# Performance work log

Measured on AMD Instinct MI355X. Metric: run time of the kernel, lower is better.

## Reference

```python
import jax, jax.numpy as jnp
import numpy as np
from jax import lax


def _conv(x, w, b=None):
    # NCHW conv, 'same' padding, stride 1
    y = lax.conv_general_dilated(x, w, (1, 1), 'SAME',
                                 dimension_numbers=('NCHW', 'OIHW', 'NCHW'))
    return y if b is None else y + b[None, :, None, None]


def _up2(x):
    # nn.Upsample(scale_factor=2), nearest
    return jnp.repeat(jnp.repeat(x, 2, axis=2), 2, axis=3)


def _rot_attn(x, wq, wk, wv, lng, lnb, reach=1):
    # Batched sliding-window rotatory cross-attention (replaces the Python loop
    # over window positions).  x: [B, C, H, W]; each position i in [reach, B-reach)
    # attends (as query) to its 2*reach neighbor frames.
    B, C, H, W = x.shape
    xs = x.reshape(B, C, H * W).transpose(0, 2, 1)          # [B, N, C]
    tgt = xs[reach:B - reach]                               # [P, N, C]
    offs = [o for o in range(-reach, reach + 1) if o != 0]  # fixed small set
    nbs = jnp.stack([xs[reach + o: B - reach + o] for o in offs], axis=1)  # [P,2r,N,C]
    q = tgt @ wq
    k = nbs @ wk
    v = nbs @ wv
    scores = jnp.einsum('pnc,pjmc->pjnm', q, k) / jnp.asarray(C, x.dtype) ** 0.5
    ctx = jnp.einsum('pjnm,pjmc->pjnc', jax.nn.softmax(scores, axis=-1), v).mean(1)  # [P,N,C]
    # LayerNorm over C
    mu = ctx.mean(-1, keepdims=True)
    var = ((ctx - mu) ** 2).mean(-1, keepdims=True)
    ctx = (ctx - mu) * lax.rsqrt(var + 1e-5) * lng + lnb
    cm = ctx.mean(0)                                        # mean over positions [N,C]
    return x + cm.T.reshape(C, H, W)[None]                  # broadcast residual


def _block(h, skip, w_up, b_up, wq, wk, wv, lng, lnb, bng, bnb, w_cb):
    h = _conv(_up2(h), w_up, b_up)                          # 1x1 conv
    h = jnp.concatenate([h, skip], axis=1)
    h = _rot_attn(h, wq, wk, wv, lng, lnb)
    # ConvolutionBatchNormblock: BN (batch stats, eps=1e-5) -> ReLU -> conv (no bias)
    mu = h.mean((0, 2, 3))
    var = ((h - mu[None, :, None, None]) ** 2).mean((0, 2, 3))
    h = (h - mu[None, :, None, None]) * lax.rsqrt(var + 1e-5)[None, :, None, None]
    h = h * bng[None, :, None, None] + bnb[None, :, None, None]
    return _conv(jax.nn.relu(h), w_cb)


def setup_inputs() -> dict:
    key = jax.random.key(0)
    ks = iter(jax.random.split(key, 64))
    n = lambda shape, s: jax.random.normal(next(ks), shape, jnp.float32) * s
    d = {}
    d['x'] = n([6, 64, 768], 1.0)
    d['skip0'] = n([6, 256, 16, 16], 1.0)
    d['skip1'] = n([6, 128, 32, 32], 1.0)
    d['skip2'] = n([6, 64, 64, 64], 1.0)
    d['w_sc'] = n([512, 768, 3, 3], 0.02)
    d['b_sc'] = jnp.zeros([512], jnp.float32)
    for i, (cin, cout) in enumerate([(512, 256), (256, 128), (128, 64)], 1):
        s = cin ** -0.5
        d[f'w_up{i}'] = n([cout, cin, 1, 1], s)
        d[f'b_up{i}'] = jnp.zeros([cout], jnp.float32)
        d[f'wq{i}'] = n([cin, cin], s)
        d[f'wk{i}'] = n([cin, cin], s)
        d[f'wv{i}'] = n([cin, cin], s)
        d[f'lng{i}'] = jnp.ones([cin], jnp.float32)
        d[f'lnb{i}'] = jnp.zeros([cin], jnp.float32)
        d[f'bng{i}'] = jnp.ones([cin], jnp.float32)
        d[f'bnb{i}'] = jnp.zeros([cin], jnp.float32)
        d[f'w_cb{i}'] = n([cout, cin, 3, 3], s * 0.3)
    return d


def reference(x, skip0, skip1, skip2, w_sc, b_sc,
              w_up1, b_up1, wq1, wk1, wv1, lng1, lnb1, bng1, bnb1, w_cb1,
              w_up2, b_up2, wq2, wk2, wv2, lng2, lnb2, bng2, bnb2, w_cb2,
              w_up3, b_up3, wq3, wk3, wv3, lng3, lnb3, bng3, bnb3, w_cb3):
    B, N, D = x.shape
    g = int(N ** 0.5)  # 8x8 token grid (image_size*2 / patch_size)
    h = _conv(x.transpose(0, 2, 1).reshape(B, D, g, g), w_sc, b_sc)   # [B,512,8,8]
    h = _block(h, skip0, w_up1, b_up1, wq1, wk1, wv1, lng1, lnb1, bng1, bnb1, w_cb1)
    h = _block(h, skip1, w_up2, b_up2, wq2, wk2, wv2, lng2, lnb2, bng2, bnb2, w_cb2)
    h = _block(h, skip2, w_up3, b_up3, wq3, wk3, wv3, lng3, lnb3, bng3, bnb3, w_cb3)
    return _up2(h)                                                    # [B,64,128,128]
```

## Files before the change

### kernel.cpp

```cpp
#include <hip/hip_runtime.h>
#include <hip/hip_bf16.h>

typedef const float* fp;
typedef unsigned short u16;
typedef __attribute__((ext_vector_type(8))) short short8v;
typedef __attribute__((ext_vector_type(4))) float f32x4;

__device__ __forceinline__ u16 f2b(float f){
  union{float f; unsigned u;} x; x.f = f;
  unsigned r = x.u + 0x7FFFu + ((x.u>>16)&1u);
  return (u16)(r>>16);
}

__global__ __launch_bounds__(256) void k_fill(float* out, int n, float v){
  int i = blockIdx.x*256 + threadIdx.x;
  if(i < n) out[i] = v;
}
__global__ __launch_bounds__(256) void k_fillb(float* out, fp bias, int Cout, int N){
  int i = blockIdx.x*256 + threadIdx.x;
  if(i < 6*Cout*N) out[i] = bias[(i/N)%Cout];
}
__global__ __launch_bounds__(256) void k_b16(fp in, u16* o, int n){
  int i = (blockIdx.x*256 + threadIdx.x)*8;
  if(i >= n) return;
  u16 tmp[8];
  #pragma unroll
  for(int e=0;e<8;e++) tmp[e] = f2b(in[i+e]);
  *(short8v*)(o+i) = *(const short8v*)tmp;
}
__global__ __launch_bounds__(256) void k_wtr(fp w, u16* wt, int Cout, int Cin){
  int idx = blockIdx.x*256 + threadIdx.x;
  int cc = Cout*Cin;
  if(idx >= 9*cc) return;
  int tap = idx / cc, rem = idx - tap*cc;
  wt[idx] = f2b(w[(size_t)rem*9 + tap]);
}
__global__ __launch_bounds__(256) void k_wqkvt(fp wq, fp wk, fp wv, u16* bt, int C, float rs){
  int idx = blockIdx.x*256 + threadIdx.x;
  if(idx >= 3*C*C) return;
  int r = idx / C, ci = idx - r*C;
  int sel = r / C, co = r - sel*C;
  float v = (sel==0 ? wq : sel==1 ? wk : wv)[(size_t)ci*C + co];
  bt[idx] = f2b(sel==0 ? v*rs : v);
}

__global__ __launch_bounds__(256) void k_in_tr(fp x, float* h0){
  int n = blockIdx.x, b = blockIdx.y;
  for(int d = threadIdx.x; d < 768; d += blockDim.x)
    h0[((size_t)b*768 + d)*64 + n] = x[((size_t)b*64 + n)*768 + d];
}

__global__ __launch_bounds__(256) void k_conv3_mfma2(const u16* __restrict__ wt,
    const u16* __restrict__ inb16, float* __restrict__ out,
    int Cin, int Cout, int H, int W, int S){
  const int N = H*W;
  __shared__ u16 As[64*40];
  __shared__ u16 Bs[64*40];
  int t = threadIdx.x, wid = t>>6, lane = t&63, l15 = lane&15, g = lane>>4;
  int b = blockIdx.z / S, s = blockIdx.z % S;
  int co0 = blockIdx.y*64, px0 = blockIdx.x*64;
  int ciN = Cin/S, ci0 = s*ciN;
  const u16* inb = inb16 + (size_t)b*Cin*N;
  int arow = t>>2, acol = (t&3)*8;
  int bpx = t&63, boct = t>>6;
  int p = px0 + bpx, py = p/W, px_ = p - py*W;
  int nc = ciN >> 5, nk = 9*nc;
  f32x4 acc[4];
  #pragma unroll
  for(int i=0;i<4;i++) acc[i] = f32x4{0.f,0.f,0.f,0.f};
  short8v av; u16 bt[8];

  #define PREF(ks) { int tap = (ks)/nc; int c0 = ((ks) - tap*nc)<<5;                     \
      int dy = tap/3 - 1, dx = tap - (tap/3)*3 - 1;                                      \
      av = *(const short8v*)(wt + ((size_t)tap*Cout + co0 + arow)*Cin + ci0 + c0 + acol);\
      bool val = ((unsigned)(py+dy) < (unsigned)H) && ((unsigned)(px_+dx) < (unsigned)W);\
      const u16* bp = inb + (size_t)(ci0 + c0 + boct*8)*N + (p + dy*W + dx);             \
      _Pragma("unroll") for(int e=0;e<8;e++) bt[e] = val ? bp[(size_t)e*N] : (u16)0; }

  PREF(0);
  for(int ks = 0; ks < nk; ks++){
    __syncthreads();
    *(short8v*)(As + arow*40 + acol) = av;
    *(short8v*)(Bs + bpx*40 + boct*8) = *(const short8v*)bt;
    __syncthreads();
    if(ks+1 < nk) PREF(ks+1);
    short8v a = *(const short8v*)(As + (wid*16+l15)*40 + 8*g);
    #pragma unroll
    for(int pt=0; pt<4; pt++){
      short8v bf = *(const short8v*)(Bs + (pt*16+l15)*40 + 8*g);
      acc[pt] = __builtin_amdgcn_mfma_f32_16x16x32_bf16(a, bf, acc[pt], 0,0,0);
    }
  }
  #undef PREF
  #pragma unroll
  for(int pt=0; pt<4; pt++){
    #pragma unroll
    for(int r=0; r<4; r++){
      size_t o = ((size_t)b*Cout + co0 + wid*16 + 4*g + r)*N + px0 + pt*16 + l15;
      if(S == 1) out[o] = acc[pt][r];
      else atomicAdd(out + o, acc[pt][r]);
    }
  }
}

__global__ __launch_bounds__(256) void k_gemm_qkv(const u16* __restrict__ XB,
    const u16* __restrict__ BT, u16* __restrict__ Qo, u16* __restrict__ Ko,
    u16* __restrict__ Vo, int C, int Nn){
  __shared__ u16 As[64*40], Bs[64*40];
  int t = threadIdx.x, wid = t>>6, lane = t&63, l15 = lane&15, g = lane>>4;
  int r0 = blockIdx.x*64, c0 = blockIdx.y*64;
  int arow = t>>2, acol = (t&3)*8;
  int nk = C/32;
  f32x4 acc[4];
  #pragma unroll
  for(int i=0;i<4;i++) acc[i] = f32x4{0.f,0.f,0.f,0.f};
  short8v av = *(const short8v*)(XB + (size_t)(r0+arow)*C + acol);
  short8v bv = *(const short8v*)(BT + (size_t)(c0+arow)*C + acol);
  for(int ks = 0; ks < nk; ks++){
    __syncthreads();
    *(short8v*)(As + arow*40 + acol) = av;
    *(short8v*)(Bs + arow*40 + acol) = bv;
    __syncthreads();
    if(ks+1 < nk){
      int k0 = (ks+1)*32;
      av = *(const short8v*)(XB + (size_t)(r0+arow)*C + k0 + acol);
      bv = *(const short8v*)(BT + (size_t)(c0+arow)*C + k0 + acol);
    }
    short8v a = *(const short8v*)(As + (wid*16+l15)*40 + 8*g);
    #pragma unroll
    for(int pt=0; pt<4; pt++){
      short8v bf = *(const short8v*)(Bs + (pt*16+l15)*40 + 8*g);
      acc[pt] = __builtin_amdgcn_mfma_f32_16x16x32_bf16(a, bf, acc[pt], 0,0,0);
    }
  }
  int sel = c0 / C, cb = c0 - sel*C;
  if(sel < 2){
    u16* ob = sel==0 ? Qo : Ko;
    #pragma unroll
    for(int pt=0; pt<4; pt++){
      #pragma unroll
      for(int r=0; r<4; r++)
        ob[(size_t)(r0 + wid*16 + 4*g + r)*C + cb + pt*16 + l15] = f2b(acc[pt][r]);
    }
  }else{
    int b = r0 / Nn, nb = r0 - b*Nn;
    #pragma unroll
    for(int pt=0; pt<4; pt++){
      #pragma unroll
      for(int r=0; r<4; r++)
        Vo[((size_t)b*C + cb + pt*16 + l15)*Nn + nb + wid*16 + 4*g + r] = f2b(acc[pt][r]);
    }
  }
}

__global__ void k_conv1_low(const float* __restrict__ in, fp w, fp bias,
                            float* __restrict__ out, int Cin, int Cout, int N1){
  int bc = blockIdx.x; int b = bc / Cout; int co = bc % Cout;
  extern __shared__ float ws[];
  for(int i = threadIdx.x; i < Cin; i += blockDim.x) ws[i] = w[(size_t)co*Cin + i];
  __syncthreads();
  const float* inb = in + (size_t)b*Cin*N1;
  float bv = bias[co];
  for(int p = threadIdx.x; p < N1; p += blockDim.x){
    float acc = bv;
    for(int ci = 0; ci < Cin; ci++) acc += inb[(size_t)ci*N1 + p] * ws[ci];
    out[((size_t)b*Cout + co)*N1 + p] = acc;
  }
}

__global__ __launch_bounds__(256) void k_concat_up(const float* __restrict__ a, fp skip,
                                                   float* __restrict__ cat,
                                                   int Ca, int Cs, int N2, int W2){
  int bc = blockIdx.x; int C = Ca + Cs; int b = bc / C; int c = bc % C;
  float* o = cat + (size_t)bc*N2;
  if(c < Ca){
    const float* s = a + ((size_t)b*Ca + c)*(N2/4);
    int W1 = W2/2;
    for(int n = threadIdx.x; n < N2; n += blockDim.x){
      int y = n / W2, x = n % W2;
      o[n] = s[(y>>1)*W1 + (x>>1)];
    }
  }else{
    fp s = skip + ((size_t)b*Cs + (c-Ca))*N2;
    for(int n = threadIdx.x; n < N2; n += blockDim.x) o[n] = s[n];
  }
}

__global__ __launch_bounds__(256) void k_trb(const float* __restrict__ src, u16* __restrict__ dst,
                                             int C, int N){
  __shared__ float tb[32][33];
  int b = blockIdx.z;
  int c0 = blockIdx.y*32, n0 = blockIdx.x*32;
  int tx = threadIdx.x & 31, ty = threadIdx.x >> 5;
  for(int i = ty; i < 32; i += 8) tb[i][tx] = src[((size_t)b*C + c0+i)*N + n0+tx];
  __syncthreads();
  for(int i = ty; i < 32; i += 8) dst[((size_t)b*N + n0+i)*C + c0+tx] = f2b(tb[tx][i]);
}

__global__ __launch_bounds__(256) void k_attn128(const u16* __restrict__ Q,
                                                 const u16* __restrict__ K,
                                                 const u16* __restrict__ VT,
                                                 float* __restrict__ ctxn, int N){
  constexpr int C = 128, KVB = 64, KP = C+8, VP = KVB+8;
  __shared__ u16 Ks[KVB*KP];
  __shared__ u16 Vt[C*VP];
  __shared__ u16 ps[4][16*VP];
  int t = threadIdx.x, wid = t>>6, lane = t&63, l15 = lane&15, g = lane>>4;
  int p = blockIdx.y, q0 = (blockIdx.x*4 + wid)*16, j = blockIdx.z;
  const u16* Qb = Q + ((size_t)(p+1)*N + q0)*C;
  const u16* Kb = K  + (size_t)(p + (j?2:0))*N*C;
  const u16* Vb = VT + (size_t)(p + (j?2:0))*C*N;
  short8v qf[4];
  #pragma unroll
  for(int kk = 0; kk < 4; kk++)
    qf[kk] = *(const short8v*)(Qb + (size_t)l15*C + kk*32 + 8*g);
  f32x4 acc[8];
  #pragma unroll
  for(int i=0;i<8;i++) acc[i] = f32x4{0.f,0.f,0.f,0.f};
  float m[4] = {-1e30f,-1e30f,-1e30f,-1e30f};
  float l[4] = {0.f,0.f,0.f,0.f};
  short8v kpre[4], vpre[4];

  #define APREF(M0) { _Pragma("unroll") for(int i=0;i<4;i++){                  \
        int idx = t*8 + i*2048; int mm = idx>>7, cc = idx&127;                 \
        kpre[i] = *(const short8v*)(Kb + (size_t)((M0)+mm)*C + cc); }          \
      _Pragma("unroll") for(int i=0;i<4;i++){                                  \
        int idx = t*8 + i*2048; int c = idx>>6, mo = idx&63;                   \
        vpre[i] = *(const short8v*)(Vb + (size_t)c*N + (M0) + mo); } }

  APREF(0);
  for(int m0 = 0; m0 < N; m0 += KVB){
    __syncthreads();
    #pragma unroll
    for(int i=0;i<4;i++){ int idx = t*8 + i*2048; int mm = idx>>7, cc = idx&127;
      *(short8v*)(Ks + mm*KP + cc) = kpre[i]; }
    #pragma unroll
    for(int i=0;i<4;i++){ int idx = t*8 + i*2048; int c = idx>>6, mo = idx&63;
      *(short8v*)(Vt + c*VP + mo) = vpre[i]; }
    __syncthreads();
    if(m0 + KVB < N) APREF(m0 + KVB);
    f32x4 s[4];
    #pragma unroll
    for(int h=0; h<4; h++){
      s[h] = f32x4{0.f,0.f,0.f,0.f};
      #pragma unroll
      for(int kk=0; kk<4; kk++){
        short8v kf = *(const short8v*)(Ks + (h*16+l15)*KP + kk*32 + 8*g);
        s[h] = __builtin_amdgcn_mfma_f32_16x16x32_bf16(qf[kk], kf, s[h], 0,0,0);
      }
    }
    float pmax[4]; bool need = false;
    #pragma unroll
    for(int r=0; r<4; r++){
      float mx = fmaxf(fmaxf(s[0][r],s[1][r]), fmaxf(s[2][r],s[3][r]));
      #pragma unroll
      for(int off=1; off<16; off<<=1) mx = fmaxf(mx, __shfl_xor(mx, off));
      pmax[r] = mx; need |= (mx > m[r] + 8.f);
    }
    if(__any((int)need)){
      #pragma unroll
      for(int r=0; r<4; r++){
        float mnew = fmaxf(m[r], pmax[r]);
        float scl = __expf(m[r] - mnew);
        l[r] *= scl; m[r] = mnew;
        #pragma unroll
        for(int ct=0; ct<8; ct++) acc[ct][r] *= scl;
      }
    }
    #pragma unroll
    for(int r=0; r<4; r++){
      float psum = 0.f;
      #pragma unroll
      for(int h=0; h<4; h++){
        float e = __expf(s[h][r] - m[r]); psum += e;
        ps[wid][(4*g+r)*VP + h*16 + l15] = f2b(e);
      }
      #pragma unroll
      for(int off=1; off<16; off<<=1) psum += __shfl_xor(psum, off);
      l[r] += psum;
    }
    #pragma unroll
    for(int ks=0; ks<2; ks++){
      short8v pa = *(const short8v*)(ps[wid] + l15*VP + ks*32 + 8*g);
      #pragma unroll
      for(int ct=0; ct<8; ct++){
        short8v vb = *(const short8v*)(Vt + (ct*16+l15)*VP + ks*32 + 8*g);
        acc[ct] = __builtin_amdgcn_mfma_f32_16x16x32_bf16(pa, vb, acc[ct], 0,0,0);
      }
    }
  }
  #undef APREF
  float inv[4];
  #pragma unroll
  for(int r=0; r<4; r++) inv[r] = 0.5f/l[r];
  #pragma unroll
  for(int ct=0; ct<8; ct++){
    int c = ct*16 + l15;
    #pragma unroll
    for(int r=0; r<4; r++)
      atomicAdd(&ctxn[((size_t)p*N + q0 + 4*g + r)*C + c], acc[ct][r]*inv[r]);
  }
}

template<int C>
__global__ __launch_bounds__(256) void k_attn_mfma(const u16* __restrict__ Q,
                                                   const u16* __restrict__ K,
                                                   const u16* __restrict__ VT,
                                                   float* __restrict__ ctxn, int N){
  constexpr int KP = C + 8;
  __shared__ u16 Ks[32*KP];
  __shared__ u16 Vt[C*40];
  __shared__ u16 ps[4][16*40];
  int t = threadIdx.x, wid = t>>6, lane = t&63;
  int l15 = lane&15, g = lane>>4;
  int p = blockIdx.y, j = blockIdx.z;
  int q0 = (blockIdx.x*4 + wid)*16;
  const u16* Qb = Q + ((size_t)(p+1)*N + q0)*C;
  const u16* Kb = K  + (size_t)(p + (j?2:0))*N*C;
  const u16* Vb = VT + (size_t)(p + (j?2:0))*C*N;

  short8v qf[C/32];
  #pragma unroll
  for(int kk = 0; kk < C/32; kk++)
    qf[kk] = *(const short8v*)(Qb + (size_t)l15*C + kk*32 + 8*g);

  f32x4 acc[C/16];
  #pragma unroll
  for(int i = 0; i < C/16; i++) acc[i] = f32x4{0.f,0.f,0.f,0.f};
  float mrow[4] = {-1e30f,-1e30f,-1e30f,-1e30f};
  float lrow[4] = {0.f,0.f,0.f,0.f};

  for(int m0 = 0; m0 < N; m0 += 32){
    __syncthreads();
    for(int idx = t*8; idx < 32*C; idx += 2048){
      int m = idx/C, c = idx - m*C;
      *(short8v*)(Ks + m*KP + c) = *(const short8v*)(Kb + (size_t)(m0+m)*C + c);
    }
    for(int idx = t*8; idx < 32*C; idx += 2048){
      int c = idx >> 5, mo = idx & 31;
      *(short8v*)(Vt + c*40 + mo) = *(const short8v*)(Vb + (size_t)c*N + m0 + mo);
    }
    __syncthreads();
    f32x4 s0 = {0.f,0.f,0.f,0.f}, s1 = {0.f,0.f,0.f,0.f};
    #pragma unroll
    for(int kk = 0; kk < C/32; kk++){
      short8v k0 = *(const short8v*)(Ks + l15*KP      + kk*32 + 8*g);
      short8v k1 = *(const short8v*)(Ks + (16+l15)*KP + kk*32 + 8*g);
      s0 = __builtin_amdgcn_mfma_f32_16x16x32_bf16(qf[kk], k0, s0, 0,0,0);
      s1 = __builtin_amdgcn_mfma_f32_16x16x32_bf16(qf[kk], k1, s1, 0,0,0);
    }
    float scl[4];
    #pragma unroll
    for(int r = 0; r < 4; r++){
      float mx = fmaxf(s0[r], s1[r]);
      #pragma unroll
      for(int off = 1; off < 16; off <<= 1) mx = fmaxf(mx, __shfl_xor(mx, off));
      float mnew = fmaxf(mrow[r], mx);
      scl[r] = __expf(mrow[r] - mnew);
      float e0 = __expf(s0[r] - mnew), e1 = __expf(s1[r] - mnew);
      float psum = e0 + e1;
      #pragma unroll
      for(int off = 1; off < 16; off <<= 1) psum += __shfl_xor(psum, off);
      lrow[r] = lrow[r]*scl[r] + psum;
      mrow[r] = mnew;
      int m = 4*g + r;
      ps[wid][m*40 + l15]      = f2b(e0);
      ps[wid][m*40 + 16 + l15] = f2b(e1);
    }
    #pragma unroll
    for(int ct = 0; ct < C/16; ct++){
      #pragma unroll
      for(int r = 0; r < 4; r++) acc[ct][r] *= scl[r];
    }
    short8v pa = *(const short8v*)(ps[wid] + l15*40 + 8*g);
    #pragma unroll
    for(int ct = 0; ct < C/16; ct++){
      short8v vb = *(const short8v*)(Vt + (ct*16+l15)*40 + 8*g);
      acc[ct] = __builtin_amdgcn_mfma_f32_16x16x32_bf16(pa, vb, acc[ct], 0,0,0);
    }
  }
  #pragma unroll
  for(int ct = 0; ct < C/16; ct++){
    int c = ct*16 + l15;
    #pragma unroll
    for(int r = 0; r < 4; r++){
      int m = 4*g + r;
      atomicAdd(&ctxn[((size_t)p*N + q0 + m)*C + c], 0.5f*acc[ct][r]/lrow[r]);
    }
  }
}

__global__ __launch_bounds__(64) void k_ln64(float* __restrict__ ctxn, fp lng, fp lnb, int C){
  float* row = ctxn + (size_t)blockIdx.x*C;
  int t = threadIdx.x;
  float s = 0.f, s2 = 0.f;
  for(int c = t; c < C; c += 64){ float v = row[c]; s += v; s2 += v*v; }
  #pragma unroll
  for(int off = 32; off > 0; off >>= 1){ s += __shfl_xor(s, off); s2 += __shfl_xor(s2, off); }
  float m = s/(float)C, var = s2/(float)C - m*m;
  float ri = rsqrtf(var + 1e-5f);
  for(int c = t; c < C; c += 64) row[c] = (row[c] - m)*ri*lng[c] + lnb[c];
}

__global__ void k_cm(const float* __restrict__ ctxn, float* __restrict__ cm, int C, int N){
  int n = blockIdx.x;
  for(int c = threadIdx.x; c < C; c += blockDim.x){
    float s = 0.25f*( ctxn[((size_t)0*N + n)*C + c] + ctxn[((size_t)1*N + n)*C + c]
                    + ctxn[((size_t)2*N + n)*C + c] + ctxn[((size_t)3*N + n)*C + c]);
    cm[(size_t)n*C + c] = s;
  }
}

__global__ __launch_bounds__(256) void k_add(float* __restrict__ h, const float* __restrict__ cm,
                                             int C, int N){
  int bc = blockIdx.x; int c = bc % C;
  float* hp = h + (size_t)bc*N;
  for(int n = threadIdx.x; n < N; n += blockDim.x) hp[n] += cm[(size_t)n*C + c];
}

__global__ __launch_bounds__(256) void k_bnstat(const float* __restrict__ h, fp bng, fp bnb,
                                                float* __restrict__ ssout, int C, int N){
  __shared__ float red[8], red2[8];
  int c = blockIdx.x; int t = threadIdx.x;
  float s = 0.f, s2 = 0.f;
  for(int b = 0; b < 6; b++){
    const float* hp = h + ((size_t)b*C + c)*N;
    for(int n = t; n < N; n += blockDim.x){ float v = hp[n]; s += v; s2 += v*v; }
  }
  for(int o = 32; o > 0; o >>= 1){ s += __shfl_down(s, o); s2 += __shfl_down(s2, o); }
  int lane = t & 63, wid = t >> 6;
  if(lane == 0){ red[wid] = s; red2[wid] = s2; }
  __syncthreads();
  if(t == 0){
    float S = 0.f, S2 = 0.f; int nw = blockDim.x >> 6;
    for(int i = 0; i < nw; i++){ S += red[i]; S2 += red2[i]; }
    float inv = 1.f/(6.f*(float)N);
    float m = S*inv, var = S2*inv - m*m;
    float sc = bng[c]*rsqrtf(var + 1e-5f);
    ssout[c] = sc; ssout[C + c] = bnb[c] - m*sc;
  }
}

__global__ __launch_bounds__(256) void k_bnrelu(float* __restrict__ h, const float* __restrict__ ssin,
                                                int C, int N){
  int bc = blockIdx.x; int c = bc % C;
  float sc = ssin[c], sh = ssin[C + c];
  float* hp = h + (size_t)bc*N;
  for(int n = threadIdx.x; n < N; n += blockDim.x){
    float v = hp[n]*sc + sh; hp[n] = v > 0.f ? v : 0.f;
  }
}

__global__ __launch_bounds__(256) void k_up_out(const float* __restrict__ in, float* out,
                                                int H, int W){
  int bc = blockIdx.x;
  const float* ip = in + (size_t)bc*H*W;
  float* op = out + (size_t)bc*4*H*W;
  int W2 = 2*W, N2 = 4*H*W;
  for(int p = threadIdx.x; p < N2; p += blockDim.x){
    int y = p / W2, x = p % W2;
    op[p] = ip[(y>>1)*W + (x>>1)];
  }
}

extern "C" void kernel_launch(void* const* d_in, const int* in_sizes, int n_in,
                              void* d_out, int out_size, void* d_ws, size_t ws_size,
                              hipStream_t stream){
  float* out_f = (float*)d_out;
  static const int EXP[36] = {294912,393216,786432,1572864,3538944,512,
    131072,256,262144,262144,262144,512,512,512,512,1179648,
    32768,128,65536,65536,65536,256,256,256,256,294912,
    8192,64,16384,16384,16384,128,128,128,128,73728};
  bool ok = (n_in == 36) && (out_size == 6291456);
  if(ok) for(int i = 0; i < 36; i++) if(in_sizes[i] != EXP[i]){ ok = false; break; }
  if(!ok){
    k_fill<<<(out_size+255)/256, 256, 0, stream>>>(out_f, out_size, 10.0f);
    return;
  }
  const size_t R = 3145728;
  const size_t NEED = (5*R + 1024)*sizeof(float);
  if(ws_size < NEED){
    k_fill<<<(out_size+255)/256, 256, 0, stream>>>(out_f, out_size, 100.0f);
    return;
  }
  (void)hipGetLastError();
  #define CKERR(code) do{ if(hipGetLastError() != hipSuccess){ \
      k_fill<<<(out_size+255)/256, 256, 0, stream>>>(out_f, out_size, (float)(code)); \
      return; } }while(0)

  fp x = (fp)d_in[0];
  fp skip[3]  = {(fp)d_in[1],(fp)d_in[2],(fp)d_in[3]};
  fp w_sc = (fp)d_in[4], b_sc = (fp)d_in[5];
  fp w_up[3] = {(fp)d_in[6], (fp)d_in[16],(fp)d_in[26]};
  fp b_up[3] = {(fp)d_in[7], (fp)d_in[17],(fp)d_in[27]};
  fp wq[3]   = {(fp)d_in[8], (fp)d_in[18],(fp)d_in[28]};
  fp wk[3]   = {(fp)d_in[9], (fp)d_in[19],(fp)d_in[29]};
  fp wv[3]   = {(fp)d_in[10],(fp)d_in[20],(fp)d_in[30]};
  fp lng[3]  = {(fp)d_in[11],(fp)d_in[21],(fp)d_in[31]};
  fp lnb[3]  = {(fp)d_in[12],(fp)d_in[22],(fp)d_in[32]};
  fp bng[3]  = {(fp)d_in[13],(fp)d_in[23],(fp)d_in[33]};
  fp bnb[3]  = {(fp)d_in[14],(fp)d_in[24],(fp)d_in[34]};
  fp w_cb[3] = {(fp)d_in[15],(fp)d_in[25],(fp)d_in[35]};

  float* Wp = (float*)d_ws;
  float *Cc = Wp, *CT = Wp + R;
  u16 *QB = (u16*)(Wp + 2*R), *KB = (u16*)(Wp + 3*R), *VB = (u16*)(Wp + 4*R);
  float *SS = Wp + 5*R;
  float *OB = Wp + R, *Bf = Wp + 2*R, *CM = Wp + 2*R;
  u16 *XB  = QB + R;
  u16 *WQT = KB + R;
  u16 *WT = KB, *IB = VB;

  k_in_tr<<<dim3(64,6),256,0,stream>>>(x, Cc);
  k_b16<<<(294912/8+255)/256, 256, 0, stream>>>(Cc, IB, 294912);
  k_wtr<<<(9*512*768+255)/256, 256, 0, stream>>>(w_sc, WT, 512, 768);
  k_fillb<<<(6*512*64+255)/256, 256, 0, stream>>>(OB, b_sc, 512, 64);
  k_conv3_mfma2<<<dim3(1,8,6*8), 256, 0, stream>>>(WT, IB, OB, 768, 512, 8, 8, 8);
  CKERR(20);

  const int Cskip[3] = {256,128,64};
  const int Hs[3]    = {16,32,64};
  const int SPL[3]   = {4,2,1};
  int Cprev = 512;
  for(int i = 0; i < 3; i++){
    int H = Hs[i], N = H*H;
    int N1 = N/4;
    int Cup = Cprev/2;
    int C = Cup + Cskip[i];
    k_conv1_low<<<6*Cup, (N1<256?N1:256), Cprev*4, stream>>>(OB, w_up[i], b_up[i], Bf, Cprev, Cup, N1);
    k_concat_up<<<6*C, 256, 0, stream>>>(Bf, skip[i], Cc, Cup, Cskip[i], N, H);
    k_trb<<<dim3(N/32, C/32, 6), 256, 0, stream>>>(Cc, XB, C, N);
    float rsv = 1.f/sqrtf((float)C);
    k_wqkvt<<<(3*C*C+255)/256, 256, 0, stream>>>(wq[i], wk[i], wv[i], WQT, C, rsv);
    k_gemm_qkv<<<dim3(6*N/64, 3*C/64), 256, 0, stream>>>(XB, WQT, QB, KB, VB, C, N);
    CKERR(30 + 10*i);
    k_fill<<<(4*N*C+255)/256, 256, 0, stream>>>(CT, 4*N*C, 0.f);
    if(i==0) k_attn_mfma<512><<<dim3(N/64,4,2),256,0,stream>>>(QB,KB,VB,CT,N);
    if(i==1) k_attn_mfma<256><<<dim3(N/64,4,2),256,0,stream>>>(QB,KB,VB,CT,N);
    if(i==2) k_attn128<<<dim3(N/64,4,2),256,0,stream>>>(QB,KB,VB,CT,N);
    k_ln64<<<4*N, 64, 0, stream>>>(CT, lng[i], lnb[i], C);
    CKERR(32 + 10*i);
    k_cm<<<N, C, 0, stream>>>(CT, CM, C, N);
    k_add<<<6*C, 256, 0, stream>>>(Cc, CM, C, N);
    k_bnstat<<<C, 256, 0, stream>>>(Cc, bng[i], bnb[i], SS, C, N);
    k_bnrelu<<<6*C, 256, 0, stream>>>(Cc, SS, C, N);
    int Co = C/2, S = SPL[i];
    k_b16<<<(6*C*N/8+255)/256, 256, 0, stream>>>(Cc, IB, 6*C*N);
    k_wtr<<<(9*Co*C+255)/256, 256, 0, stream>>>(w_cb[i], WT, Co, C);
    if(S > 1) k_fill<<<(6*Co*N+255)/256, 256, 0, stream>>>(OB, 6*Co*N, 0.f);
    k_conv3_mfma2<<<dim3(N/64, Co/64, 6*S), 256, 0, stream>>>(WT, IB, OB, C, Co, H, H, S);
    CKERR(34 + 10*i);
    Cprev = Co;
  }
  k_up_out<<<6*64, 256, 0, stream>>>(OB, out_f, 64, 64);
  CKERR(90);
  #undef CKERR
}
```

Baseline: 809.9 us.

## Fuse residual add with BN stats, fuse BN-ReLU with bf16 cast, tune attn128

The residual add now also accumulates per-channel BN sums through atomics, and a tiny kernel finalizes scale and shift. The BN+ReLU kernel writes the bf16 conv input directly, which removes a separate read pass over the activation. In the C=128 attention kernel, the row-max shuffle reduction runs only when rescaling is needed, the row-sum reduction is deferred to the end, s_setprio brackets the MFMA sections, and the P scratch is re-padded. The deferred max reduction relies on the any-lane check to keep lanes consistent, and the atomics make the statistics order nondeterministic.

```diff
diff --git a/kernel.cpp b/kernel.cpp
--- a/kernel.cpp
+++ b/kernel.cpp
@@ -201,10 +201,10 @@
                                                  const u16* __restrict__ K,
                                                  const u16* __restrict__ VT,
                                                  float* __restrict__ ctxn, int N){
-  constexpr int C = 128, KVB = 64, KP = C+8, VP = KVB+8;
+  constexpr int C = 128, KVB = 64, KP = C+8, VP = KVB+8, PSP = 68;
   __shared__ u16 Ks[KVB*KP];
   __shared__ u16 Vt[C*VP];
-  __shared__ u16 ps[4][16*VP];
+  __shared__ u16 ps[4][16*PSP];
   int t = threadIdx.x, wid = t>>6, lane = t&63, l15 = lane&15, g = lane>>4;
   int p = blockIdx.y, q0 = (blockIdx.x*4 + wid)*16, j = blockIdx.z;
   const u16* Qb = Q + ((size_t)(p+1)*N + q0)*C;
@@ -240,6 +240,7 @@
     __syncthreads();
     if(m0 + KVB < N) APREF(m0 + KVB);
     f32x4 s[4];
+    __builtin_amdgcn_s_setprio(1);
     #pragma unroll
     for(int h=0; h<4; h++){
       s[h] = f32x4{0.f,0.f,0.f,0.f};
@@ -249,18 +250,20 @@
         s[h] = __builtin_amdgcn_mfma_f32_16x16x32_bf16(qf[kk], kf, s[h], 0,0,0);
       }
     }
-    float pmax[4]; bool need = false;
+    __builtin_amdgcn_s_setprio(0);
+    float lmax[4]; bool need = false;
     #pragma unroll
     for(int r=0; r<4; r++){
-      float mx = fmaxf(fmaxf(s[0][r],s[1][r]), fmaxf(s[2][r],s[3][r]));
-      #pragma unroll
-      for(int off=1; off<16; off<<=1) mx = fmaxf(mx, __shfl_xor(mx, off));
-      pmax[r] = mx; need |= (mx > m[r] + 8.f);
+      float a = fmaxf(fmaxf(s[0][r],s[1][r]), fmaxf(s[2][r],s[3][r]));
+      lmax[r] = a; need |= (a > m[r] + 8.f);
     }
     if(__any((int)need)){
       #pragma unroll
       for(int r=0; r<4; r++){
-        float mnew = fmaxf(m[r], pmax[r]);
+        float mx = lmax[r];
+        #pragma unroll
+        for(int off=1; off<16; off<<=1) mx = fmaxf(mx, __shfl_xor(mx, off));
+        float mnew = fmaxf(m[r], mx);
         float scl = __expf(m[r] - mnew);
         l[r] *= scl; m[r] = mnew;
         #pragma unroll
@@ -269,30 +272,35 @@
     }
     #pragma unroll
     for(int r=0; r<4; r++){
-      float psum = 0.f;
+      float ls = 0.f;
       #pragma unroll
       for(int h=0; h<4; h++){
-        float e = __expf(s[h][r] - m[r]); psum += e;
-        ps[wid][(4*g+r)*VP + h*16 + l15] = f2b(e);
+        float e = __expf(s[h][r] - m[r]); ls += e;
+        ps[wid][(4*g+r)*PSP + h*16 + l15] = f2b(e);
       }
-      #pragma unroll
-      for(int off=1; off<16; off<<=1) psum += __shfl_xor(psum, off);
-      l[r] += psum;
-    }
+      l[r] += ls;
+    }
+    __builtin_amdgcn_s_setprio(1);
     #pragma unroll
     for(int ks=0; ks<2; ks++){
-      short8v pa = *(const short8v*)(ps[wid] + l15*VP + ks*32 + 8*g);
+      short8v pa = *(const short8v*)(ps[wid] + l15*PSP + ks*32 + 8*g);
       #pragma unroll
       for(int ct=0; ct<8; ct++){
         short8v vb = *(const short8v*)(Vt + (ct*16+l15)*VP + ks*32 + 8*g);
         acc[ct] = __builtin_amdgcn_mfma_f32_16x16x32_bf16(pa, vb, acc[ct], 0,0,0);
       }
     }
+    __builtin_amdgcn_s_setprio(0);
   }
   #undef APREF
   float inv[4];
   #pragma unroll
-  for(int r=0; r<4; r++) inv[r] = 0.5f/l[r];
+  for(int r=0; r<4; r++){
+    float lr = l[r];
+    #pragma unroll
+    for(int off=1; off<16; off<<=1) lr += __shfl_xor(lr, off);
+    inv[r] = 0.5f/lr;
+  }
   #pragma unroll
   for(int ct=0; ct<8; ct++){
     int c = ct*16 + l15;
@@ -411,43 +419,40 @@
   }
 }
 
-__global__ __launch_bounds__(256) void k_add(float* __restrict__ h, const float* __restrict__ cm,
-                                             int C, int N){
+__global__ __launch_bounds__(256) void k_addstat(float* __restrict__ h, const float* __restrict__ cm,
+                                                 float* __restrict__ ss2, int C, int N){
   int bc = blockIdx.x; int c = bc % C;
   float* hp = h + (size_t)bc*N;
-  for(int n = threadIdx.x; n < N; n += blockDim.x) hp[n] += cm[(size_t)n*C + c];
-}
-
-__global__ __launch_bounds__(256) void k_bnstat(const float* __restrict__ h, fp bng, fp bnb,
-                                                float* __restrict__ ssout, int C, int N){
-  __shared__ float red[8], red2[8];
-  int c = blockIdx.x; int t = threadIdx.x;
   float s = 0.f, s2 = 0.f;
-  for(int b = 0; b < 6; b++){
-    const float* hp = h + ((size_t)b*C + c)*N;
-    for(int n = t; n < N; n += blockDim.x){ float v = hp[n]; s += v; s2 += v*v; }
-  }
+  for(int n = threadIdx.x; n < N; n += blockDim.x){
+    float v = hp[n] + cm[(size_t)n*C + c];
+    hp[n] = v; s += v; s2 += v*v;
+  }
+  #pragma unroll
   for(int o = 32; o > 0; o >>= 1){ s += __shfl_down(s, o); s2 += __shfl_down(s2, o); }
-  int lane = t & 63, wid = t >> 6;
-  if(lane == 0){ red[wid] = s; red2[wid] = s2; }
-  __syncthreads();
-  if(t == 0){
-    float S = 0.f, S2 = 0.f; int nw = blockDim.x >> 6;
-    for(int i = 0; i < nw; i++){ S += red[i]; S2 += red2[i]; }
-    float inv = 1.f/(6.f*(float)N);
-    float m = S*inv, var = S2*inv - m*m;
-    float sc = bng[c]*rsqrtf(var + 1e-5f);
-    ssout[c] = sc; ssout[C + c] = bnb[c] - m*sc;
-  }
-}
-
-__global__ __launch_bounds__(256) void k_bnrelu(float* __restrict__ h, const float* __restrict__ ssin,
-                                                int C, int N){
+  if((threadIdx.x & 63) == 0){
+    atomicAdd(&ss2[c], s); atomicAdd(&ss2[C + c], s2);
+  }
+}
+__global__ void k_bnfin(const float* __restrict__ ss2, fp bng, fp bnb,
+                        float* __restrict__ ss, int C, int N){
+  int c = threadIdx.x;
+  if(c >= C) return;
+  float inv = 1.f/(6.f*(float)N);
+  float m = ss2[c]*inv, var = ss2[C+c]*inv - m*m;
+  float sc = bng[c]*rsqrtf(var + 1e-5f);
+  ss[c] = sc; ss[C + c] = bnb[c] - m*sc;
+}
+
+__global__ __launch_bounds__(256) void k_bnrelu2(float* __restrict__ h, const float* __restrict__ ssin,
+                                                 u16* __restrict__ ob, int C, int N){
   int bc = blockIdx.x; int c = bc % C;
   float sc = ssin[c], sh = ssin[C + c];
   float* hp = h + (size_t)bc*N;
+  u16* op = ob + (size_t)bc*N;
   for(int n = threadIdx.x; n < N; n += blockDim.x){
-    float v = hp[n]*sc + sh; hp[n] = v > 0.f ? v : 0.f;
+    float v = hp[n]*sc + sh; v = v > 0.f ? v : 0.f;
+    hp[n] = v; op[n] = f2b(v);
   }
 }
 
@@ -478,7 +483,7 @@
     return;
   }
   const size_t R = 3145728;
-  const size_t NEED = (5*R + 1024)*sizeof(float);
+  const size_t NEED = (5*R + 4096)*sizeof(float);
   if(ws_size < NEED){
     k_fill<<<(out_size+255)/256, 256, 0, stream>>>(out_f, out_size, 100.0f);
     return;
@@ -505,7 +510,8 @@
   float* Wp = (float*)d_ws;
   float *Cc = Wp, *CT = Wp + R;
   u16 *QB = (u16*)(Wp + 2*R), *KB = (u16*)(Wp + 3*R), *VB = (u16*)(Wp + 4*R);
-  float *SS = Wp + 5*R;
+  float *SS  = Wp + 5*R;
+  float *SS2 = Wp + 5*R + 2048;
   float *OB = Wp + R, *Bf = Wp + 2*R, *CM = Wp + 2*R;
   u16 *XB  = QB + R;
   u16 *WQT = KB + R;
@@ -541,11 +547,11 @@
     k_ln64<<<4*N, 64, 0, stream>>>(CT, lng[i], lnb[i], C);
     CKERR(32 + 10*i);
     k_cm<<<N, C, 0, stream>>>(CT, CM, C, N);
-    k_add<<<6*C, 256, 0, stream>>>(Cc, CM, C, N);
-    k_bnstat<<<C, 256, 0, stream>>>(Cc, bng[i], bnb[i], SS, C, N);
-    k_bnrelu<<<6*C, 256, 0, stream>>>(Cc, SS, C, N);
+    k_fill<<<(2*C+255)/256, 256, 0, stream>>>(SS2, 2*C, 0.f);
+    k_addstat<<<6*C, 256, 0, stream>>>(Cc, CM, SS2, C, N);
+    k_bnfin<<<1, C, 0, stream>>>(SS2, bng[i], bnb[i], SS, C, N);
+    k_bnrelu2<<<6*C, 256, 0, stream>>>(Cc, SS, IB, C, N);
     int Co = C/2, S = SPL[i];
-    k_b16<<<(6*C*N/8+255)/256, 256, 0, stream>>>(Cc, IB, 6*C*N);
     k_wtr<<<(9*Co*C+255)/256, 256, 0, stream>>>(w_cb[i], WT, Co, C);
     if(S > 1) k_fill<<<(6*Co*N+255)/256, 256, 0, stream>>>(OB, 6*Co*N, 0.f);
     k_conv3_mfma2<<<dim3(N/64, Co/64, 6*S), 256, 0, stream>>>(WT, IB, OB, C, Co, H, H, S);
```

Result: faster. 751.4 us (-7.2%).
